# Performance work log

Hardware: AMD Instinct MI355X
Metric: run time of the kernel (lower is better)

## Reference

```python
import jax, jax.numpy as jnp
import numpy as np

THETA = 10000.0

def apply_rope(x, positions):
    # x: [B, H, S, d_k], positions: [S] int
    d_k = x.shape[-1]
    inv_freq = THETA ** (-jnp.arange(0, d_k, 2, dtype=jnp.float32) / d_k)  # [d_k/2]
    ang = positions.astype(jnp.float32)[:, None] * inv_freq[None, :]        # [S, d_k/2]
    cos, sin = jnp.cos(ang), jnp.sin(ang)
    x_even = x[..., 0::2]
    x_odd = x[..., 1::2]
    r_even = x_even * cos - x_odd * sin
    r_odd = x_even * sin + x_odd * cos
    # interleave back
    return jnp.stack([r_even, r_odd], axis=-1).reshape(x.shape)

def setup_inputs() -> dict:
    key = jax.random.key(0)
    k1, k2, k3 = jax.random.split(key, 3)
    B, S, D = 2, 2048, 1024
    x = jax.random.normal(k1, (B, S, D), dtype=jnp.float32)
    token_positions = jnp.arange(S, dtype=jnp.int32)
    W_qkv = jax.random.normal(k2, (3 * D, D), dtype=jnp.float32) * 0.02
    W_o = jax.random.normal(k3, (D, D), dtype=jnp.float32) * 0.02
    return {"x": x, "token_positions": token_positions, "W_qkv": W_qkv, "W_o": W_o}

def reference(x, token_positions, W_qkv, W_o):
    B, S, D = x.shape
    H = 16
    d_k = D // H
    qkv = jnp.einsum('bsd,ed->bse', x, W_qkv)           # [B, S, 3D]
    q, k, v = jnp.split(qkv, 3, axis=-1)
    def to_heads(t):
        return t.reshape(B, S, H, d_k).transpose(0, 2, 1, 3)  # [B, H, S, d_k]
    hq, hk, hv = to_heads(q), to_heads(k), to_heads(v)
    hq = apply_rope(hq, token_positions)
    hk = apply_rope(hk, token_positions)
    scale = d_k ** -0.5
    scores = jnp.einsum('bhqd,bhkd->bhqk', hq, hk) * scale  # [B, H, S, S]
    causal = jnp.tril(jnp.ones((S, S), dtype=bool))
    scores = jnp.where(causal, scores, -jnp.inf)
    attn = jax.nn.softmax(scores, axis=-1)
    out = jnp.einsum('bhqk,bhkd->bhqd', attn, hv)           # [B, H, S, d_k]
    out = out.transpose(0, 2, 1, 3).reshape(B, S, D)
    return jnp.einsum('bsd,ed->bse', out, W_o)
```

## Files before the change

### kernel.cpp

```cpp
#include <hip/hip_runtime.h>
#include <math.h>

typedef short short8 __attribute__((ext_vector_type(8)));
typedef float f32x4 __attribute__((ext_vector_type(4)));
typedef unsigned int u32x2 __attribute__((ext_vector_type(2)));

typedef __attribute__((address_space(1))) const void* as1p;
typedef __attribute__((address_space(3))) void* as3p;

__device__ __forceinline__ unsigned short f2bf(float f) {
    unsigned int u = __float_as_uint(f);
    u += 0x7fffu + ((u >> 16) & 1u);
    return (unsigned short)(u >> 16);
}

__global__ void cvt_all_bf16(const float* __restrict__ x,
                             const float* __restrict__ wqkv,
                             const float* __restrict__ wo,
                             unsigned short* __restrict__ xb,
                             unsigned short* __restrict__ wqkvb,
                             unsigned short* __restrict__ wob) {
    int i = blockIdx.x * blockDim.x + threadIdx.x;
    const float* src;
    unsigned short* dst;
    int off;
    if (i < 1048576)       { src = x;    dst = xb;    off = i; }
    else if (i < 1835008)  { src = wqkv; dst = wqkvb; off = i - 1048576; }
    else                   { src = wo;   dst = wob;   off = i - 1835008; }
    float4 v = ((const float4*)src)[off];
    ushort4 o = make_ushort4(f2bf(v.x), f2bf(v.y), f2bf(v.z), f2bf(v.w));
    ((ushort4*)dst)[off] = o;
}

template <int RF, int NTX, bool BF16_OUT, bool DO_ROPE>
__global__ __launch_bounds__(256) void gemm_nt_mfma(
    const unsigned short* __restrict__ A, const unsigned short* __restrict__ B,
    void* __restrict__ Cv, const int* __restrict__ pos, int N, int K) {
    constexpr int BM = RF * 32;
    __shared__ unsigned short As[BM * 32];
    __shared__ unsigned short Bs[128 * 32];
    const int tid = threadIdx.x;
    const int wave = tid >> 6, lane = tid & 63;
    const int L = blockIdx.x;
    const int xcd = L & 7, idx = L >> 3;
    const int nt_ = xcd * NTX + idx % NTX;
    const int mt  = idx / NTX;
    const int m0 = mt * BM, n0 = nt_ << 7;
    const int wr = ((wave >> 1) & 1) * (RF * 16);
    const int wc = (wave & 1) << 6;

    const int r0 = tid >> 2;
    const int ko = (((tid & 3) ^ ((r0 >> 1) & 3)) << 3);
    const unsigned short* Ap0 = A + (size_t)(m0 + r0) * K + ko;
    const unsigned short* Ap1 = A + (size_t)(m0 + (RF == 4 ? 64 : 0) + r0) * K + ko;
    const unsigned short* Bp0 = B + (size_t)(n0 + r0) * K + ko;
    const unsigned short* Bp1 = B + (size_t)(n0 + 64 + r0) * K + ko;

    f32x4 acc[RF][4] = {};
    const int lro = lane & 15;
    const int cs = ((lane >> 4) ^ ((lro >> 1) & 3)) << 3;

    for (int k0 = 0; k0 < K; k0 += 32) {
        __syncthreads();
        __builtin_amdgcn_global_load_lds((as1p)(Ap0 + k0), (as3p)(As + tid * 8), 16, 0, 0);
        if constexpr (RF == 4)
            __builtin_amdgcn_global_load_lds((as1p)(Ap1 + k0), (as3p)(As + (256 + tid) * 8), 16, 0, 0);
        __builtin_amdgcn_global_load_lds((as1p)(Bp0 + k0), (as3p)(Bs + tid * 8), 16, 0, 0);
        __builtin_amdgcn_global_load_lds((as1p)(Bp1 + k0), (as3p)(Bs + (256 + tid) * 8), 16, 0, 0);
        __syncthreads();

        short8 af[RF], bfr[4];
        #pragma unroll
        for (int i = 0; i < RF; i++) af[i] = *(const short8*)&As[(wr + i * 16 + lro) * 32 + cs];
        #pragma unroll
        for (int j = 0; j < 4; j++) bfr[j] = *(const short8*)&Bs[(wc + j * 16 + lro) * 32 + cs];
        #pragma unroll
        for (int i = 0; i < RF; i++)
            #pragma unroll
            for (int j = 0; j < 4; j++)
                acc[i][j] = __builtin_amdgcn_mfma_f32_16x16x32_bf16(af[i], bfr[j], acc[i][j], 0, 0, 0);
    }

    const int row_b = m0 + wr + ((lane >> 4) << 2);
    const int col_b = n0 + wc + lro;

    if constexpr (DO_ROPE) {
        const int sec = (n0 + wc) >> 10;
        if (sec < 2) {
            const float qs = (sec == 0) ? 0.18033688011112042f : 1.0f;
            const float sgn = (lane & 1) ? 1.0f : -1.0f;
            float ps[RF * 4];
            #pragma unroll
            for (int i = 0; i < RF; i++)
                #pragma unroll
                for (int r = 0; r < 4; r++)
                    ps[i * 4 + r] = (float)pos[(row_b + i * 16 + r) & 2047];
            #pragma unroll
            for (int j = 0; j < 4; j++) {
                float invf_rev = exp2f(-(float)((lro >> 1) + 8 * j) * 0.41524101186092029f)
                                 * 0.15915494309189535f;
                #pragma unroll
                for (int i = 0; i < RF; i++)
                    #pragma unroll
                    for (int r = 0; r < 4; r++) {
                        float rev = ps[i * 4 + r] * invf_rev;
                        rev -= floorf(rev);
                        float c = __builtin_amdgcn_cosf(rev) * qs;
                        float s = __builtin_amdgcn_sinf(rev) * (qs * sgn);
                        float mine = acc[i][j][r];
                        float partner = __shfl_xor(mine, 1, 64);
                        acc[i][j][r] = mine * c + partner * s;
                    }
            }
        }
    }

    #pragma unroll
    for (int i = 0; i < RF; i++)
        #pragma unroll
        for (int j = 0; j < 4; j++)
            #pragma unroll
            for (int r = 0; r < 4; r++) {
                size_t idx2 = (size_t)(row_b + i * 16 + r) * N + (col_b + j * 16);
                if constexpr (BF16_OUT) ((unsigned short*)Cv)[idx2] = f2bf(acc[i][j][r]);
                else ((float*)Cv)[idx2] = acc[i][j][r];
            }
}

__global__ __launch_bounds__(256) void flash_attn_mfma(
    const unsigned short* __restrict__ qkv, unsigned short* __restrict__ Ows) {
    const int S = 2048, D3 = 3072;
    const int L = blockIdx.x + (blockIdx.y << 4) + (blockIdx.z << 8);
    const int xcd = L & 7, t = L >> 3;
    const int pp = t & 15;
    const int g2 = xcd + ((t >> 4) << 3);
    const int h = g2 & 15, b = g2 >> 4;
    const int tid = threadIdx.x, wave = tid >> 6, lane = tid & 63;
    const int lro = lane & 15, grp = lane >> 4;

    __shared__ __align__(16) unsigned short Ks[2][64 * 64];
    __shared__ __align__(16) unsigned int   Vp[2][64 * 34];
    __shared__ float RedW[4][16][66];
    __shared__ float Lbuf[4][4][16];

    const int sr = tid >> 3;
    const int sc = ((tid & 7) ^ (sr & 7)) << 3;
    const int m = tid >> 3;
    const int vo = (tid & 7) << 3;

    const int Rk = (wave << 4) + lro;
    const int koffA = Rk * 64 + ((grp ^ (lro & 7)) << 3);
    const int koffB = Rk * 64 + (((grp ^ 4) ^ (lro & 7)) << 3);
    const int vcb = (wave << 3) + (grp << 1);
    const int klb = (wave << 4) + (grp << 2);

    const unsigned short* kbg = qkv + (size_t)(b * S) * D3 + 1024 + h * 64;
    const unsigned short* vbg = qkv + (size_t)(b * S) * D3 + 2048 + h * 64;

    for (int ph = 0; ph < 2; ph++) {
        const int qt = ph ? 31 - pp : pp;
        const int q0 = qt << 6;
        const int nkt = qt + 1;

        __syncthreads();

        short8 bq[4][2];
        #pragma unroll
        for (int f = 0; f < 4; f++) {
            const unsigned short* qrow =
                qkv + (size_t)(b * S + q0 + f * 16 + lro) * D3 + h * 64 + grp * 8;
            bq[f][0] = *(const short8*)qrow;
            bq[f][1] = *(const short8*)(qrow + 32);
        }

        __builtin_amdgcn_global_load_lds((as1p)(kbg + (size_t)sr * D3 + sc),
                                         (as3p)&Ks[0][tid * 8], 16, 0, 0);
        __builtin_amdgcn_global_load_lds((as1p)(kbg + (size_t)(sr + 32) * D3 + sc),
                                         (as3p)&Ks[0][(tid + 256) * 8], 16, 0, 0);
        {
            const unsigned short* vs = vbg + (size_t)(2 * m) * D3 + vo;
            uint4 va = *(const uint4*)vs;
            uint4 vb = *(const uint4*)(vs + (size_t)D3);
            const unsigned short* pa_ = (const unsigned short*)&va;
            const unsigned short* pb_ = (const unsigned short*)&vb;
            #pragma unroll
            for (int j = 0; j < 8; j++)
                Vp[0][(vo + j) * 34 + m] = (unsigned)pa_[j] | ((unsigned)pb_[j] << 16);
        }
        __syncthreads();

        f32x4 acc[4][4] = {};
        float lsum[4] = {0.f, 0.f, 0.f, 0.f};

        for (int kt = 0; kt < nkt; kt++) {
            const int cur = kt & 1, nxt = cur ^ 1;
            const bool pf = (kt + 1 < nkt);
            uint4 va, vb;
            if (pf) {
                const unsigned short* kb1 = kbg + (size_t)((kt + 1) * 64) * D3;
                __builtin_amdgcn_global_load_lds((as1p)(kb1 + (size_t)sr * D3 + sc),
                                                 (as3p)&Ks[nxt][tid * 8], 16, 0, 0);
                __builtin_amdgcn_global_load_lds((as1p)(kb1 + (size_t)(sr + 32) * D3 + sc),
                                                 (as3p)&Ks[nxt][(tid + 256) * 8], 16, 0, 0);
                const unsigned short* vs =
                    vbg + (size_t)((kt + 1) * 64 + 2 * m) * D3 + vo;
                va = *(const uint4*)vs;
                vb = *(const uint4*)(vs + (size_t)D3);
            }

            short8 ak0 = *(const short8*)&Ks[cur][koffA];
            short8 ak1 = *(const short8*)&Ks[cur][koffB];
            f32x4 s0 = {}, s1 = {}, s2 = {}, s3 = {};
            s0 = __builtin_amdgcn_mfma_f32_16x16x32_bf16(ak0, bq[0][0], s0, 0, 0, 0);
            s0 = __builtin_amdgcn_mfma_f32_16x16x32_bf16(ak1, bq[0][1], s0, 0, 0, 0);
            s1 = __builtin_amdgcn_mfma_f32_16x16x32_bf16(ak0, bq[1][0], s1, 0, 0, 0);
            s1 = __builtin_amdgcn_mfma_f32_16x16x32_bf16(ak1, bq[1][1], s1, 0, 0, 0);
            s2 = __builtin_amdgcn_mfma_f32_16x16x32_bf16(ak0, bq[2][0], s2, 0, 0, 0);
            s2 = __builtin_amdgcn_mfma_f32_16x16x32_bf16(ak1, bq[2][1], s2, 0, 0, 0);
            s3 = __builtin_amdgcn_mfma_f32_16x16x32_bf16(ak0, bq[3][0], s3, 0, 0, 0);
            s3 = __builtin_amdgcn_mfma_f32_16x16x32_bf16(ak1, bq[3][1], s3, 0, 0, 0);
            f32x4 sf[4] = {s0, s1, s2, s3};

            const bool dg = (kt == nkt - 1);
            u32x2 pw[4];
            #pragma unroll
            for (int f = 0; f < 4; f++) {
                float v0 = sf[f][0], v1 = sf[f][1], v2 = sf[f][2], v3 = sf[f][3];
                if (dg) {
                    int thr = (f << 4) + lro - klb;
                    if (0 > thr) v0 = -1e30f;
                    if (1 > thr) v1 = -1e30f;
                    if (2 > thr) v2 = -1e30f;
                    if (3 > thr) v3 = -1e30f;
                }
                float p0 = __builtin_amdgcn_exp2f(v0);
                float p1 = __builtin_amdgcn_exp2f(v1);
                float p2 = __builtin_amdgcn_exp2f(v2);
                float p3 = __builtin_amdgcn_exp2f(v3);
                lsum[f] += (p0 + p1) + (p2 + p3);
                unsigned u0, u1;
                asm("v_cvt_pk_bf16_f32 %0, %1, %2" : "=v"(u0) : "v"(p0), "v"(p1));
                asm("v_cvt_pk_bf16_f32 %0, %1, %2" : "=v"(u1) : "v"(p2), "v"(p3));
                pw[f][0] = u0;
                pw[f][1] = u1;
            }

            u32x2 vv[4];
            #pragma unroll
            for (int nt = 0; nt < 4; nt++)
                vv[nt] = *(const u32x2*)&Vp[cur][(nt * 16 + lro) * 34 + vcb];

            #pragma unroll
            for (int f = 0; f < 4; f++)
                #pragma unroll
                for (int nt = 0; nt < 4; nt++)
                    asm("v_mfma_f32_16x16x16_bf16 %0, %1, %2, %0"
                        : "+v"(acc[f][nt]) : "v"(pw[f]), "v"(vv[nt]));

            if (pf) {
                const unsigned short* pa_ = (const unsigned short*)&va;
                const unsigned short* pb_ = (const unsigned short*)&vb;
                #pragma unroll
                for (int j = 0; j < 8; j++)
                    Vp[nxt][(vo + j) * 34 + m] = (unsigned)pa_[j] | ((unsigned)pb_[j] << 16);
            }
            __syncthreads();
        }

        #pragma unroll
        for (int f = 0; f < 4; f++) {
            lsum[f] += __shfl_xor(lsum[f], 16, 64);
            lsum[f] += __shfl_xor(lsum[f], 32, 64);
        }
        if (lane < 16) {
            #pragma unroll
            for (int f = 0; f < 4; f++) Lbuf[wave][f][lro] = lsum[f];
        }

        #pragma unroll
        for (int f = 0; f < 4; f++) {
            __syncthreads();
            if (wave != f) {
                #pragma unroll
                for (int nt = 0; nt < 4; nt++)
                    #pragma unroll
                    for (int r = 0; r < 4; r++)
                        RedW[wave][(grp << 2) + r][nt * 16 + lro] = acc[f][nt][r];
            }
            __syncthreads();
            if (wave == f) {
                #pragma unroll
                for (int w2 = 0; w2 < 4; w2++) {
                    if (w2 == f) continue;
                    #pragma unroll
                    for (int nt = 0; nt < 4; nt++)
                        #pragma unroll
                        for (int r = 0; r < 4; r++)
                            acc[f][nt][r] += RedW[w2][(grp << 2) + r][nt * 16 + lro];
                }
                #pragma unroll
                for (int r = 0; r < 4; r++) {
                    int q = (grp << 2) + r;
                    float lt = Lbuf[0][f][q] + Lbuf[1][f][q] +
                               Lbuf[2][f][q] + Lbuf[3][f][q];
                    float inv = 1.0f / lt;
                    int row = q0 + (f << 4) + q;
                    #pragma unroll
                    for (int nt = 0; nt < 4; nt++)
                        Ows[(size_t)(b * S + row) * 1024 + h * 64 + nt * 16 + lro] =
                            f2bf(acc[f][nt][r] * inv);
                }
            }
        }
    }
}

extern "C" void kernel_launch(void* const* d_in, const int* in_sizes, int n_in,
                              void* d_out, int out_size, void* d_ws, size_t ws_size,
                              hipStream_t stream) {
    const float* x    = (const float*)d_in[0];
    const int*   pos  = (const int*)d_in[1];
    const float* Wqkv = (const float*)d_in[2];
    const float* Wo   = (const float*)d_in[3];
    float* out = (float*)d_out;

    unsigned short* xb    = (unsigned short*)d_ws;
    unsigned short* Wqkvb = xb + (size_t)4096 * 1024;
    unsigned short* Wob   = Wqkvb + (size_t)3072 * 1024;
    unsigned short* qkvb  = Wob + (size_t)1024 * 1024;
    unsigned short* Owsb  = qkvb + (size_t)4096 * 3072;

    cvt_all_bf16<<<8192, 256, 0, stream>>>(x, Wqkv, Wo, xb, Wqkvb, Wob);

    gemm_nt_mfma<4, 3, true, true><<<768, 256, 0, stream>>>(
        xb, Wqkvb, qkvb, pos, 3072, 1024);

    flash_attn_mfma<<<dim3(16, 16, 2), 256, 0, stream>>>(qkvb, Owsb);

    gemm_nt_mfma<2, 1, false, false><<<512, 256, 0, stream>>>(
        Owsb, Wob, out, nullptr, 1024, 1024);
}
```

Measured before the change: 185.0 us.

## Make flash attention waves load private K/V slices and drop per-tile barriers

After: 196.0 us. +5.9%, slower.

```diff
diff --git a/kernel.cpp b/kernel.cpp
--- a/kernel.cpp
+++ b/kernel.cpp
@@ -127,189 +127,171 @@
             }
 }
 
-__global__ __launch_bounds__(256) void flash_attn_mfma(
+__global__ __launch_bounds__(256, 3) void flash_attn_mfma(
     const unsigned short* __restrict__ qkv, unsigned short* __restrict__ Ows) {
     const int S = 2048, D3 = 3072;
-    const int L = blockIdx.x + (blockIdx.y << 4) + (blockIdx.z << 8);
-    const int xcd = L & 7, t = L >> 3;
-    const int pp = t & 15;
-    const int g2 = xcd + ((t >> 4) << 3);
+    const int L = blockIdx.x;
+    const int xcd = L & 7, rr = L >> 3;
+    const int qt = 31 - (rr >> 2);
+    const int g2 = xcd + ((rr & 3) << 3);
     const int h = g2 & 15, b = g2 >> 4;
     const int tid = threadIdx.x, wave = tid >> 6, lane = tid & 63;
     const int lro = lane & 15, grp = lane >> 4;
 
-    __shared__ __align__(16) unsigned short Ks[2][64 * 64];
-    __shared__ __align__(16) unsigned int   Vp[2][64 * 34];
+    __shared__ __align__(16) unsigned int Vp[64 * 34];
     __shared__ float RedW[4][16][66];
     __shared__ float Lbuf[4][4][16];
 
-    const int sr = tid >> 3;
-    const int sc = ((tid & 7) ^ (sr & 7)) << 3;
-    const int m = tid >> 3;
-    const int vo = (tid & 7) << 3;
-
-    const int Rk = (wave << 4) + lro;
-    const int koffA = Rk * 64 + ((grp ^ (lro & 7)) << 3);
-    const int koffB = Rk * 64 + (((grp ^ 4) ^ (lro & 7)) << 3);
-    const int vcb = (wave << 3) + (grp << 1);
+    const int kp = lane >> 3;
+    const int vo = (lane & 7) << 3;
+    const int wcb = wave << 3;
     const int klb = (wave << 4) + (grp << 2);
 
     const unsigned short* kbg = qkv + (size_t)(b * S) * D3 + 1024 + h * 64;
     const unsigned short* vbg = qkv + (size_t)(b * S) * D3 + 2048 + h * 64;
 
-    for (int ph = 0; ph < 2; ph++) {
-        const int qt = ph ? 31 - pp : pp;
-        const int q0 = qt << 6;
-        const int nkt = qt + 1;
-
+    const int q0 = qt << 6;
+    const int nkt = qt + 1;
+
+    short8 bq[4][2];
+    #pragma unroll
+    for (int f = 0; f < 4; f++) {
+        const unsigned short* qrow =
+            qkv + (size_t)(b * S + q0 + f * 16 + lro) * D3 + h * 64 + grp * 8;
+        bq[f][0] = *(const short8*)qrow;
+        bq[f][1] = *(const short8*)(qrow + 32);
+    }
+
+    const unsigned short* kfp = kbg + (size_t)(16 * wave + lro) * D3 + grp * 8;
+    const unsigned short* vfp = vbg + (size_t)(16 * wave + 2 * kp) * D3 + vo;
+
+    short8 kc0 = *(const short8*)kfp;
+    short8 kc1 = *(const short8*)(kfp + 32);
+    {
+        uint4 va = *(const uint4*)vfp;
+        uint4 vb = *(const uint4*)(vfp + D3);
+        const unsigned short* pa_ = (const unsigned short*)&va;
+        const unsigned short* pb_ = (const unsigned short*)&vb;
+        #pragma unroll
+        for (int j = 0; j < 8; j++)
+            Vp[(vo + j) * 34 + wcb + kp] = (unsigned)pa_[j] | ((unsigned)pb_[j] << 16);
+    }
+
+    f32x4 acc[4][4] = {};
+    float lsum[4] = {0.f, 0.f, 0.f, 0.f};
+
+    for (int kt = 0; kt < nkt; kt++) {
+        const bool pf = (kt + 1 < nkt);
+        short8 kn0, kn1;
+        uint4 vna, vnb;
+        if (pf) {
+            const size_t off = (size_t)((kt + 1) * 64) * D3;
+            kn0 = *(const short8*)(kfp + off);
+            kn1 = *(const short8*)(kfp + off + 32);
+            vna = *(const uint4*)(vfp + off);
+            vnb = *(const uint4*)(vfp + off + D3);
+        }
+
+        f32x4 s0 = {}, s1 = {}, s2 = {}, s3 = {};
+        s0 = __builtin_amdgcn_mfma_f32_16x16x32_bf16(kc0, bq[0][0], s0, 0, 0, 0);
+        s0 = __builtin_amdgcn_mfma_f32_16x16x32_bf16(kc1, bq[0][1], s0, 0, 0, 0);
+        s1 = __builtin_amdgcn_mfma_f32_16x16x32_bf16(kc0, bq[1][0], s1, 0, 0, 0);
+        s1 = __builtin_amdgcn_mfma_f32_16x16x32_bf16(kc1, bq[1][1], s1, 0, 0, 0);
+        s2 = __builtin_amdgcn_mfma_f32_16x16x32_bf16(kc0, bq[2][0], s2, 0, 0, 0);
+        s2 = __builtin_amdgcn_mfma_f32_16x16x32_bf16(kc1, bq[2][1], s2, 0, 0, 0);
+        s3 = __builtin_amdgcn_mfma_f32_16x16x32_bf16(kc0, bq[3][0], s3, 0, 0, 0);
+        s3 = __builtin_amdgcn_mfma_f32_16x16x32_bf16(kc1, bq[3][1], s3, 0, 0, 0);
+        f32x4 sf[4] = {s0, s1, s2, s3};
+
+        const bool dg = (kt == nkt - 1);
+        u32x2 pw[4];
+        #pragma unroll
+        for (int f = 0; f < 4; f++) {
+            float v0 = sf[f][0], v1 = sf[f][1], v2 = sf[f][2], v3 = sf[f][3];
+            if (dg) {
+                int thr = (f << 4) + lro - klb;
+                if (0 > thr) v0 = -1e30f;
+                if (1 > thr) v1 = -1e30f;
+                if (2 > thr) v2 = -1e30f;
+                if (3 > thr) v3 = -1e30f;
+            }
+            float p0 = __builtin_amdgcn_exp2f(v0);
+            float p1 = __builtin_amdgcn_exp2f(v1);
+            float p2 = __builtin_amdgcn_exp2f(v2);
+            float p3 = __builtin_amdgcn_exp2f(v3);
+            lsum[f] += (p0 + p1) + (p2 + p3);
+            unsigned u0, u1;
+            asm("v_cvt_pk_bf16_f32 %0, %1, %2" : "=v"(u0) : "v"(p0), "v"(p1));
+            asm("v_cvt_pk_bf16_f32 %0, %1, %2" : "=v"(u1) : "v"(p2), "v"(p3));
+            pw[f][0] = u0;
+            pw[f][1] = u1;
+        }
+
+        u32x2 vv[4];
+        #pragma unroll
+        for (int nt = 0; nt < 4; nt++)
+            vv[nt] = *(const u32x2*)&Vp[(nt * 16 + lro) * 34 + wcb + (grp << 1)];
+
+        #pragma unroll
+        for (int f = 0; f < 4; f++)
+            #pragma unroll
+            for (int nt = 0; nt < 4; nt++)
+                asm("v_mfma_f32_16x16x16_bf16 %0, %1, %2, %0"
+                    : "+v"(acc[f][nt]) : "v"(pw[f]), "v"(vv[nt]));
+
+        if (pf) {
+            const unsigned short* pa_ = (const unsigned short*)&vna;
+            const unsigned short* pb_ = (const unsigned short*)&vnb;
+            #pragma unroll
+            for (int j = 0; j < 8; j++)
+                Vp[(vo + j) * 34 + wcb + kp] = (unsigned)pa_[j] | ((unsigned)pb_[j] << 16);
+            kc0 = kn0;
+            kc1 = kn1;
+        }
+    }
+
+    #pragma unroll
+    for (int f = 0; f < 4; f++) {
+        lsum[f] += __shfl_xor(lsum[f], 16, 64);
+        lsum[f] += __shfl_xor(lsum[f], 32, 64);
+    }
+    if (lane < 16) {
+        #pragma unroll
+        for (int f = 0; f < 4; f++) Lbuf[wave][f][lro] = lsum[f];
+    }
+
+    #pragma unroll
+    for (int f = 0; f < 4; f++) {
         __syncthreads();
-
-        short8 bq[4][2];
-        #pragma unroll
-        for (int f = 0; f < 4; f++) {
-            const unsigned short* qrow =
-                qkv + (size_t)(b * S + q0 + f * 16 + lro) * D3 + h * 64 + grp * 8;
-            bq[f][0] = *(const short8*)qrow;
-            bq[f][1] = *(const short8*)(qrow + 32);
-        }
-
-        __builtin_amdgcn_global_load_lds((as1p)(kbg + (size_t)sr * D3 + sc),
-                                         (as3p)&Ks[0][tid * 8], 16, 0, 0);
-        __builtin_amdgcn_global_load_lds((as1p)(kbg + (size_t)(sr + 32) * D3 + sc),
-                                         (as3p)&Ks[0][(tid + 256) * 8], 16, 0, 0);
-        {
-            const unsigned short* vs = vbg + (size_t)(2 * m) * D3 + vo;
-            uint4 va = *(const uint4*)vs;
-            uint4 vb = *(const uint4*)(vs + (size_t)D3);
-            const unsigned short* pa_ = (const unsigned short*)&va;
-            const unsigned short* pb_ = (const unsigned short*)&vb;
-            #pragma unroll
-            for (int j = 0; j < 8; j++)
-                Vp[0][(vo + j) * 34 + m] = (unsigned)pa_[j] | ((unsigned)pb_[j] << 16);
+        if (wave != f) {
+            #pragma unroll
+            for (int nt = 0; nt < 4; nt++)
+                #pragma unroll
+                for (int r = 0; r < 4; r++)
+                    RedW[wave][(grp << 2) + r][nt * 16 + lro] = acc[f][nt][r];
         }
         __syncthreads();
-
-        f32x4 acc[4][4] = {};
-        float lsum[4] = {0.f, 0.f, 0.f, 0.f};
-
-        for (int kt = 0; kt < nkt; kt++) {
-            const int cur = kt & 1, nxt = cur ^ 1;
-            const bool pf = (kt + 1 < nkt);
-            uint4 va, vb;
-            if (pf) {
-                const unsigned short* kb1 = kbg + (size_t)((kt + 1) * 64) * D3;
-                __builtin_amdgcn_global_load_lds((as1p)(kb1 + (size_t)sr * D3 + sc),
-                                                 (as3p)&Ks[nxt][tid * 8], 16, 0, 0);
-                __builtin_amdgcn_global_load_lds((as1p)(kb1 + (size_t)(sr + 32) * D3 + sc),
-                                                 (as3p)&Ks[nxt][(tid + 256) * 8], 16, 0, 0);
-                const unsigned short* vs =
-                    vbg + (size_t)((kt + 1) * 64 + 2 * m) * D3 + vo;
-                va = *(const uint4*)vs;
-                vb = *(const uint4*)(vs + (size_t)D3);
-            }
-
-            short8 ak0 = *(const short8*)&Ks[cur][koffA];
-            short8 ak1 = *(const short8*)&Ks[cur][koffB];
-            f32x4 s0 = {}, s1 = {}, s2 = {}, s3 = {};
-            s0 = __builtin_amdgcn_mfma_f32_16x16x32_bf16(ak0, bq[0][0], s0, 0, 0, 0);
-            s0 = __builtin_amdgcn_mfma_f32_16x16x32_bf16(ak1, bq[0][1], s0, 0, 0, 0);
-            s1 = __builtin_amdgcn_mfma_f32_16x16x32_bf16(ak0, bq[1][0], s1, 0, 0, 0);
-            s1 = __builtin_amdgcn_mfma_f32_16x16x32_bf16(ak1, bq[1][1], s1, 0, 0, 0);
-            s2 = __builtin_amdgcn_mfma_f32_16x16x32_bf16(ak0, bq[2][0], s2, 0, 0, 0);
-            s2 = __builtin_amdgcn_mfma_f32_16x16x32_bf16(ak1, bq[2][1], s2, 0, 0, 0);
-            s3 = __builtin_amdgcn_mfma_f32_16x16x32_bf16(ak0, bq[3][0], s3, 0, 0, 0);
-            s3 = __builtin_amdgcn_mfma_f32_16x16x32_bf16(ak1, bq[3][1], s3, 0, 0, 0);
-            f32x4 sf[4] = {s0, s1, s2, s3};
-
-            const bool dg = (kt == nkt - 1);
-            u32x2 pw[4];
-            #pragma unroll
-            for (int f = 0; f < 4; f++) {
-                float v0 = sf[f][0], v1 = sf[f][1], v2 = sf[f][2], v3 = sf[f][3];
-                if (dg) {
-                    int thr = (f << 4) + lro - klb;
-                    if (0 > thr) v0 = -1e30f;
-                    if (1 > thr) v1 = -1e30f;
-                    if (2 > thr) v2 = -1e30f;
-                    if (3 > thr) v3 = -1e30f;
-                }
-                float p0 = __builtin_amdgcn_exp2f(v0);
-                float p1 = __builtin_amdgcn_exp2f(v1);
-                float p2 = __builtin_amdgcn_exp2f(v2);
-                float p3 = __builtin_amdgcn_exp2f(v3);
-                lsum[f] += (p0 + p1) + (p2 + p3);
-                unsigned u0, u1;
-                asm("v_cvt_pk_bf16_f32 %0, %1, %2" : "=v"(u0) : "v"(p0), "v"(p1));
-                asm("v_cvt_pk_bf16_f32 %0, %1, %2" : "=v"(u1) : "v"(p2), "v"(p3));
-                pw[f][0] = u0;
-                pw[f][1] = u1;
-            }
-
-            u32x2 vv[4];
-            #pragma unroll
-            for (int nt = 0; nt < 4; nt++)
-                vv[nt] = *(const u32x2*)&Vp[cur][(nt * 16 + lro) * 34 + vcb];
-
-            #pragma unroll
-            for (int f = 0; f < 4; f++)
-                #pragma unroll
-                for (int nt = 0; nt < 4; nt++)
-                    asm("v_mfma_f32_16x16x16_bf16 %0, %1, %2, %0"
-                        : "+v"(acc[f][nt]) : "v"(pw[f]), "v"(vv[nt]));
-
-            if (pf) {
-                const unsigned short* pa_ = (const unsigned short*)&va;
-                const unsigned short* pb_ = (const unsigned short*)&vb;
-                #pragma unroll
-                for (int j = 0; j < 8; j++)
-                    Vp[nxt][(vo + j) * 34 + m] = (unsigned)pa_[j] | ((unsigned)pb_[j] << 16);
-            }
-            __syncthreads();
-        }
-
-        #pragma unroll
-        for (int f = 0; f < 4; f++) {
-            lsum[f] += __shfl_xor(lsum[f], 16, 64);
-            lsum[f] += __shfl_xor(lsum[f], 32, 64);
-        }
-        if (lane < 16) {
-            #pragma unroll
-            for (int f = 0; f < 4; f++) Lbuf[wave][f][lro] = lsum[f];
-        }
-
-        #pragma unroll
-        for (int f = 0; f < 4; f++) {
-            __syncthreads();
-            if (wave != f) {
+        if (wave == f) {
+            #pragma unroll
+            for (int w2 = 0; w2 < 4; w2++) {
+                if (w2 == f) continue;
                 #pragma unroll
                 for (int nt = 0; nt < 4; nt++)
                     #pragma unroll
                     for (int r = 0; r < 4; r++)
-                        RedW[wave][(grp << 2) + r][nt * 16 + lro] = acc[f][nt][r];
-            }
-            __syncthreads();
-            if (wave == f) {
-                #pragma unroll
-                for (int w2 = 0; w2 < 4; w2++) {
-                    if (w2 == f) continue;
-                    #pragma unroll
-                    for (int nt = 0; nt < 4; nt++)
-                        #pragma unroll
-                        for (int r = 0; r < 4; r++)
-                            acc[f][nt][r] += RedW[w2][(grp << 2) + r][nt * 16 + lro];
-                }
-                #pragma unroll
-                for (int r = 0; r < 4; r++) {
-                    int q = (grp << 2) + r;
-                    float lt = Lbuf[0][f][q] + Lbuf[1][f][q] +
-                               Lbuf[2][f][q] + Lbuf[3][f][q];
-                    float inv = 1.0f / lt;
-                    int row = q0 + (f << 4) + q;
-                    #pragma unroll
-                    for (int nt = 0; nt < 4; nt++)
-                        Ows[(size_t)(b * S + row) * 1024 + h * 64 + nt * 16 + lro] =
-                            f2bf(acc[f][nt][r] * inv);
-                }
+                        acc[f][nt][r] += RedW[w2][(grp << 2) + r][nt * 16 + lro];
+            }
+            #pragma unroll
+            for (int r = 0; r < 4; r++) {
+                int q = (grp << 2) + r;
+                float lt = Lbuf[0][f][q] + Lbuf[1][f][q] +
+                           Lbuf[2][f][q] + Lbuf[3][f][q];
+                float inv = 1.0f / lt;
+                int row = q0 + (f << 4) + q;
+                #pragma unroll
+                for (int nt = 0; nt < 4; nt++)
+                    Ows[(size_t)(b * S + row) * 1024 + h * 64 + nt * 16 + lro] =
+                        f2bf(acc[f][nt][r] * inv);
             }
         }
     }
@@ -335,7 +317,7 @@
     gemm_nt_mfma<4, 3, true, true><<<768, 256, 0, stream>>>(
         xb, Wqkvb, qkvb, pos, 3072, 1024);
 
-    flash_attn_mfma<<<dim3(16, 16, 2), 256, 0, stream>>>(qkvb, Owsb);
+    flash_attn_mfma<<<1024, 256, 0, stream>>>(qkvb, Owsb);
 
     gemm_nt_mfma<2, 1, false, false><<<512, 256, 0, stream>>>(
         Owsb, Wob, out, nullptr, 1024, 1024);
```
